# Performance work log

Hardware: AMD Instinct MI355X
Metric: run time of the kernel (lower is better)

Reference implementation:

```python
import jax, jax.numpy as jnp
import numpy as np

B, C_IN, C_OUT, N, T = 32, 64, 64, 1024, 16


def setup_inputs() -> dict:
    key = jax.random.key(0)
    k1, k2, k3, k4, k5 = jax.random.split(key, 5)
    x = jax.random.normal(k1, (B, C_IN, N, T), dtype=jnp.float32)
    adj = jax.random.uniform(k2, (N, N), dtype=jnp.float32)
    alpha = jax.random.normal(k3, (C_IN,), dtype=jnp.float32) * 0.1
    W_att = jax.random.normal(k4, (T, T), dtype=jnp.float32) * 0.1
    W_out = jax.random.normal(k5, (C_OUT, C_IN), dtype=jnp.float32) * 0.1
    return {"x": x, "adj": adj, "alpha": alpha, "W_att": W_att, "W_out": W_out}


def reference(x, adj, alpha, W_att, W_out):
    # x: [B, C_in, N, T]; adj: [N, N]
    # k = q = einsum('bint,i->bnt', x, alpha)
    k = jnp.einsum('bint,i->bnt', x, alpha)              # [B, N, T]
    # scores = k @ W @ q^T over timestep dim -> [B, N, N]
    scores = jnp.einsum('bnt,ts,bms->bnm', k, W_att, k)
    att = jax.nn.softmax(scores, axis=-1) * adj          # [B, N, N]
    # out = (att @ x.permute(3,0,2,1)) @ W_out.T, then permute back
    agg = jnp.einsum('bnm,bcmt->bcnt', att, x)           # [B, C_in, N, T]
    out = jnp.einsum('bcnt,oc->bont', agg, W_out)        # [B, C_out, N, T]
    return out
```

## Files before the change

### kernel.cpp

```cpp
#include <hip/hip_runtime.h>
#include <hip/hip_bf16.h>


typedef float  f32x4 __attribute__((ext_vector_type(4)));
typedef short  s16x8 __attribute__((ext_vector_type(8)));
typedef unsigned short u16x8 __attribute__((ext_vector_type(8)));

#define GLOAD_LDS16(g, l) __builtin_amdgcn_global_load_lds(                    \
    (const __attribute__((address_space(1))) void*)(g),                        \
    (__attribute__((address_space(3))) void*)(l), 16, 0, 0)

static __device__ __forceinline__ unsigned short f2bf(float f) {
    __hip_bfloat16 h = __float2bfloat16(f);
    return *reinterpret_cast<unsigned short*>(&h);
}

__global__ __launch_bounds__(256) void kCM(const float* __restrict__ x,
                                           const float* __restrict__ Wout,
                                           const float* __restrict__ alpha,
                                           const float* __restrict__ Watt,
                                           unsigned short* __restrict__ Yt,
                                           float* __restrict__ kk_,
                                           float* __restrict__ kq_) {
    extern __shared__ char sm[];
    float* xt = (float*)sm;
    unsigned short* Ys = (unsigned short*)sm;
    unsigned short* Wb = (unsigned short*)(sm + 66560);
    float* al = (float*)(sm + 75776);
    float* wl = (float*)(sm + 76032);
    float* kl = (float*)(sm + 77120);
    int tid = threadIdx.x;
    int b  = blockIdx.x >> 6;
    int mc = blockIdx.x & 63;
    int j0 = mc << 8;
    int m0 = mc << 4;
    if (tid < 64) al[tid] = alpha[tid];
    wl[(tid >> 4) * 17 + (tid & 15)] = Watt[tid];
    #pragma unroll
    for (int it = 0; it < 16; ++it) {
        int idx = it * 256 + tid;
        Wb[(idx >> 6) * 72 + (idx & 63)] = f2bf(Wout[idx]);
    }
    const float* xb = x + (size_t)b * (64 * 16384) + j0;
    #pragma unroll
    for (int it = 0; it < 16; ++it) {
        int idx = it * 256 + tid;
        int c = idx >> 6, j4 = (idx & 63) << 2;
        float4 v = *(const float4*)(xb + (size_t)c * 16384 + j4);
        *(float4*)&xt[c * 260 + j4] = v;
    }
    __syncthreads();
    int w = tid >> 6, l = tid & 63;
    int l15 = l & 15, lhi = l >> 4;
    int jw = w << 6;
    f32x4 acc[4][4] = {};
    s16x8 af[4][2];
    #pragma unroll
    for (int fro = 0; fro < 4; ++fro)
        #pragma unroll
        for (int ks = 0; ks < 2; ++ks)
            af[fro][ks] = *(const s16x8*)&Wb[(fro * 16 + l15) * 72 + ks * 32 + lhi * 8];
    #pragma unroll
    for (int fc = 0; fc < 4; ++fc) {
        #pragma unroll
        for (int ks = 0; ks < 2; ++ks) {
            int jcol = jw + fc * 16 + l15;
            int cb = ks * 32 + lhi * 8;
            s16x8 bf;
            #pragma unroll
            for (int e = 0; e < 8; ++e)
                bf[e] = (short)f2bf(xt[(cb + e) * 260 + jcol]);
            #pragma unroll
            for (int fro = 0; fro < 4; ++fro)
                acc[fro][fc] = __builtin_amdgcn_mfma_f32_16x16x32_bf16(
                    af[fro][ks], bf, acc[fro][fc], 0, 0, 0);
        }
    }
    {
        float kv = 0.f;
        #pragma unroll
        for (int c = 0; c < 64; ++c) kv = fmaf(al[c], xt[c * 260 + tid], kv);
        kl[tid] = kv;
        kk_[(size_t)b * 16384 + j0 + tid] = kv;
    }
    __syncthreads();
    {
        int ml = tid >> 4, tq = tid & 15;
        float q = 0.f;
        #pragma unroll
        for (int s = 0; s < 16; ++s) q = fmaf(kl[ml * 16 + s], wl[s * 17 + tq], q);
        kq_[(size_t)b * 16384 + j0 + tid] = q;
    }
    #pragma unroll
    for (int fro = 0; fro < 4; ++fro)
        #pragma unroll
        for (int fc = 0; fc < 4; ++fc) {
            int jl = jw + fc * 16 + l15;
            int o0 = fro * 16 + lhi * 4;
            ushort4 pk = make_ushort4(f2bf(acc[fro][fc][0]), f2bf(acc[fro][fc][1]),
                                      f2bf(acc[fro][fc][2]), f2bf(acc[fro][fc][3]));
            *(ushort4*)&Ys[jl * 72 + o0] = pk;
        }
    __syncthreads();
    #pragma unroll
    for (int it = 0; it < 4; ++it) {
        int r = it * 256 + tid;
        int o = r >> 4, t = r & 15;
        u16x8 v0, v1;
        #pragma unroll
        for (int q = 0; q < 8; ++q) {
            v0[q] = Ys[(q * 16 + t) * 72 + o];
            v1[q] = Ys[((q + 8) * 16 + t) * 72 + o];
        }
        unsigned short* dst = Yt + (((size_t)b << 10) + r) * 1024 + m0;
        *(u16x8*)dst = v0;
        *(u16x8*)(dst + 8) = v1;
    }
}

__global__ __launch_bounds__(256) void kBP(const float* __restrict__ kk_,
                                           const float* __restrict__ kq_,
                                           const float* __restrict__ adj,
                                           unsigned short* __restrict__ Pbf) {
    int tid = threadIdx.x;
    int b  = blockIdx.x >> 8;
    int n0 = (blockIdx.x & 255) * 4;
    __shared__ float kql[4][16];
    __shared__ float redm[4][4], reds[4][4];
    if (tid < 64)
        kql[tid >> 4][tid & 15] =
            kq_[((size_t)b * 1024 + n0 + (tid >> 4)) * 16 + (tid & 15)];
    __syncthreads();
    const float* kb = kk_ + (size_t)b * 16384;
    float kf[4][16];
    #pragma unroll
    for (int u = 0; u < 4; ++u) {
        const float* p = &kb[(size_t)(u * 256 + tid) * 16];
        #pragma unroll
        for (int s = 0; s < 16; ++s) kf[u][s] = p[s];
    }
    float sc[4][4];
    #pragma unroll
    for (int r = 0; r < 4; ++r)
        #pragma unroll
        for (int u = 0; u < 4; ++u) {
            float a = 0.f;
            #pragma unroll
            for (int s = 0; s < 16; ++s) a = fmaf(kql[r][s], kf[u][s], a);
            sc[r][u] = a;
        }
    float mx[4];
    #pragma unroll
    for (int r = 0; r < 4; ++r)
        mx[r] = fmaxf(fmaxf(sc[r][0], sc[r][1]), fmaxf(sc[r][2], sc[r][3]));
    #pragma unroll
    for (int off = 32; off; off >>= 1)
        #pragma unroll
        for (int r = 0; r < 4; ++r) mx[r] = fmaxf(mx[r], __shfl_xor(mx[r], off));
    int w = tid >> 6;
    if ((tid & 63) == 0)
        #pragma unroll
        for (int r = 0; r < 4; ++r) redm[w][r] = mx[r];
    __syncthreads();
    #pragma unroll
    for (int r = 0; r < 4; ++r)
        mx[r] = fmaxf(fmaxf(redm[0][r], redm[1][r]), fmaxf(redm[2][r], redm[3][r]));
    float e[4][4], se[4];
    #pragma unroll
    for (int r = 0; r < 4; ++r) {
        float s = 0.f;
        #pragma unroll
        for (int u = 0; u < 4; ++u) { e[r][u] = __expf(sc[r][u] - mx[r]); s += e[r][u]; }
        se[r] = s;
    }
    #pragma unroll
    for (int off = 32; off; off >>= 1)
        #pragma unroll
        for (int r = 0; r < 4; ++r) se[r] += __shfl_xor(se[r], off);
    if ((tid & 63) == 0)
        #pragma unroll
        for (int r = 0; r < 4; ++r) reds[w][r] = se[r];
    __syncthreads();
    float rrs[4];
    #pragma unroll
    for (int r = 0; r < 4; ++r)
        rrs[r] = 1.f / (reds[0][r] + reds[1][r] + reds[2][r] + reds[3][r]);
    #pragma unroll
    for (int r = 0; r < 4; ++r)
        #pragma unroll
        for (int u = 0; u < 4; ++u) {
            size_t m = (size_t)u * 256 + tid;
            float av = adj[(size_t)(n0 + r) * 1024 + m];
            Pbf[((size_t)b * 1024 + n0 + r) * 1024 + m] = f2bf(e[r][u] * rrs[r] * av);
        }
}

static __device__ __forceinline__ void stage32(const unsigned short* Pb,
                                               const unsigned short* Yb,
                                               unsigned short* lds, int buf,
                                               int kt, int ww, int l) {
    int S  = ((l >> 2) ^ (l >> 4)) & 3;
    int cs = (((l & 3) ^ S)) << 3;
    int k0 = kt << 5;
    unsigned short* base = lds + buf * 16384;
    #pragma unroll
    for (int s = 0; s < 2; ++s) {
        int rbase = s * 128 + ww * 16;
        size_t g = ((size_t)(rbase + (l >> 2)) << 10) + k0 + cs;
        GLOAD_LDS16(Pb + g, base + rbase * 32);
        GLOAD_LDS16(Yb + g, base + 8192 + rbase * 32);
    }
}

static __device__ __forceinline__ s16x8 frag32(const unsigned short* base,
                                               int row, int l) {
    int S = (row ^ (row >> 2)) & 3;
    int g = (l >> 4) & 3;
    return *(const s16x8*)(base + row * 32 + ((g ^ S) << 3));
}

__global__ __launch_bounds__(512, 2) void kD(const unsigned short* __restrict__ P,
                                             const unsigned short* __restrict__ Yt,
                                             float* __restrict__ out) {
    extern __shared__ unsigned short lds[];
    int bid = blockIdx.x;
    int wg  = (bid & 7) * 64 + (bid >> 3);
    int b   = wg >> 4;
    int rem = wg & 15;
    int n0  = (rem & 3) << 8;
    int j0  = (rem >> 2) << 8;
    int tid = threadIdx.x;
    int l = tid & 63, ww = tid >> 6;
    int wr = ww >> 2, wc = ww & 3;
    int l15 = l & 15, lhi = l >> 4;
    const unsigned short* Pb = P  + ((size_t)b << 20) + ((size_t)n0 << 10);
    const unsigned short* Yb = Yt + ((size_t)b << 20) + ((size_t)j0 << 10);

    f32x4 acc[8][4] = {};
    stage32(Pb, Yb, lds, 0, 0, ww, l);
    stage32(Pb, Yb, lds, 1, 1, ww, l);

    for (int kt = 0; kt < 32; ++kt) {
        int cur = kt % 3;
        const unsigned short* Ab = lds + cur * 16384;
        const unsigned short* Bb = Ab + 8192;
        if (kt < 31) asm volatile("s_waitcnt vmcnt(4)" ::: "memory");
        else         asm volatile("s_waitcnt vmcnt(0)" ::: "memory");
        __builtin_amdgcn_s_barrier();
        s16x8 bf[4], af0[4];
        #pragma unroll
        for (int nj = 0; nj < 4; ++nj)
            bf[nj] = frag32(Bb, wc * 64 + nj * 16 + l15, l);
        #pragma unroll
        for (int mi = 0; mi < 4; ++mi)
            af0[mi] = frag32(Ab, wr * 128 + mi * 16 + l15, l);
        if (kt < 30) stage32(Pb, Yb, lds, (kt + 2) % 3, kt + 2, ww, l);
        __builtin_amdgcn_s_barrier();
        asm volatile("s_waitcnt lgkmcnt(0)" ::: "memory");
        __builtin_amdgcn_sched_barrier(0);
        __builtin_amdgcn_s_setprio(1);
        #pragma unroll
        for (int mi = 0; mi < 4; ++mi)
            #pragma unroll
            for (int nj = 0; nj < 4; ++nj)
                acc[mi][nj] = __builtin_amdgcn_mfma_f32_16x16x32_bf16(
                    af0[mi], bf[nj], acc[mi][nj], 0, 0, 0);
        __builtin_amdgcn_s_setprio(0);
        __builtin_amdgcn_s_barrier();
        s16x8 af1[4];
        #pragma unroll
        for (int mi = 0; mi < 4; ++mi)
            af1[mi] = frag32(Ab, wr * 128 + (4 + mi) * 16 + l15, l);
        asm volatile("s_waitcnt lgkmcnt(0)" ::: "memory");
        __builtin_amdgcn_sched_barrier(0);
        __builtin_amdgcn_s_setprio(1);
        #pragma unroll
        for (int mi = 0; mi < 4; ++mi)
            #pragma unroll
            for (int nj = 0; nj < 4; ++nj)
                acc[4 + mi][nj] = __builtin_amdgcn_mfma_f32_16x16x32_bf16(
                    af1[mi], bf[nj], acc[4 + mi][nj], 0, 0, 0);
        __builtin_amdgcn_s_setprio(0);
    }

    #pragma unroll
    for (int mi = 0; mi < 8; ++mi)
        #pragma unroll
        for (int nj = 0; nj < 4; ++nj) {
            int o  = (j0 >> 4) + wc * 4 + nj;
            int nb = n0 + wr * 128 + mi * 16 + lhi * 4;
            float* op = out + ((size_t)(b * 64 + o) << 14) + (size_t)nb * 16 + l15;
            #pragma unroll
            for (int q = 0; q < 4; ++q) op[q * 16] = acc[mi][nj][q];
        }
}

extern "C" void kernel_launch(void* const* d_in, const int* in_sizes, int n_in,
                              void* d_out, int out_size, void* d_ws, size_t ws_size,
                              hipStream_t stream) {
    const float* x     = (const float*)d_in[0];
    const float* adj   = (const float*)d_in[1];
    const float* alpha = (const float*)d_in[2];
    const float* Watt  = (const float*)d_in[3];
    const float* Wout  = (const float*)d_in[4];
    float* out = (float*)d_out;

    char* ws = (char*)d_ws;
    float* k  = (float*)ws;
    float* kq = (float*)(ws + 2097152);
    unsigned short* Pbf = (unsigned short*)(ws + 4194304);
    unsigned short* Yt  = (unsigned short*)(ws + 4194304 + 67108864);

    kCM<<<2048, 256, 78144, stream>>>(x, Wout, alpha, Watt, Yt, k, kq);
    kBP<<<8192, 256, 0, stream>>>(k, kq, adj, Pbf);
    kD <<<512, 512, 98304, stream>>>(Pbf, Yt, out);
}
```

Baseline: 202.0 us.

## Store x as bf16 in LDS in kCM and switch kD to double-buffered K=64 tiles

kCM now converts x to bf16 once while loading it into LDS and accumulates the alpha-weighted k sum during the load. This shrinks shared memory so three blocks fit per CU, and the later conversion and 64-step reduction loop are gone. kD moves from a 3-stage pipeline with K=32 tiles to a 2-buffer scheme with K=64 tiles, a new XOR swizzle, and the next tile's load issued early in each iteration. LDS use in kD grows to 128KB, and the shallower pipeline may expose more load latency.

```diff
diff --git a/kernel.cpp b/kernel.cpp
--- a/kernel.cpp
+++ b/kernel.cpp
@@ -15,25 +15,27 @@
     return *reinterpret_cast<unsigned short*>(&h);
 }
 
-__global__ __launch_bounds__(256) void kCM(const float* __restrict__ x,
-                                           const float* __restrict__ Wout,
-                                           const float* __restrict__ alpha,
-                                           const float* __restrict__ Watt,
-                                           unsigned short* __restrict__ Yt,
-                                           float* __restrict__ kk_,
-                                           float* __restrict__ kq_) {
+__global__ __launch_bounds__(256, 3) void kCM(const float* __restrict__ x,
+                                              const float* __restrict__ Wout,
+                                              const float* __restrict__ alpha,
+                                              const float* __restrict__ Watt,
+                                              unsigned short* __restrict__ Yt,
+                                              float* __restrict__ kk_,
+                                              float* __restrict__ kq_) {
     extern __shared__ char sm[];
-    float* xt = (float*)sm;
-    unsigned short* Ys = (unsigned short*)sm;
-    unsigned short* Wb = (unsigned short*)(sm + 66560);
-    float* al = (float*)(sm + 75776);
-    float* wl = (float*)(sm + 76032);
-    float* kl = (float*)(sm + 77120);
+    unsigned short* xtb = (unsigned short*)sm;
+    unsigned short* Ys  = (unsigned short*)sm;
+    unsigned short* Wb  = (unsigned short*)(sm + 36864);
+    float* al   = (float*)(sm + 46080);
+    float* wl   = (float*)(sm + 46336);
+    float* kl   = (float*)(sm + 47424);
+    float* kred = (float*)(sm + 48448);
     int tid = threadIdx.x;
     int b  = blockIdx.x >> 6;
     int mc = blockIdx.x & 63;
     int j0 = mc << 8;
     int m0 = mc << 4;
+    int g = tid >> 6, lane = tid & 63;
     if (tid < 64) al[tid] = alpha[tid];
     wl[(tid >> 4) * 17 + (tid & 15)] = Watt[tid];
     #pragma unroll
@@ -41,49 +43,56 @@
         int idx = it * 256 + tid;
         Wb[(idx >> 6) * 72 + (idx & 63)] = f2bf(Wout[idx]);
     }
+    __syncthreads();
     const float* xb = x + (size_t)b * (64 * 16384) + j0;
+    float kp[4] = {0.f, 0.f, 0.f, 0.f};
     #pragma unroll
     for (int it = 0; it < 16; ++it) {
-        int idx = it * 256 + tid;
-        int c = idx >> 6, j4 = (idx & 63) << 2;
-        float4 v = *(const float4*)(xb + (size_t)c * 16384 + j4);
-        *(float4*)&xt[c * 260 + j4] = v;
-    }
-    __syncthreads();
-    int w = tid >> 6, l = tid & 63;
-    int l15 = l & 15, lhi = l >> 4;
-    int jw = w << 6;
-    f32x4 acc[4][4] = {};
-    s16x8 af[4][2];
+        int c = it * 4 + g;
+        float4 v = *(const float4*)(xb + (size_t)c * 16384 + lane * 4);
+        float a = al[c];
+        kp[0] = fmaf(a, v.x, kp[0]);
+        kp[1] = fmaf(a, v.y, kp[1]);
+        kp[2] = fmaf(a, v.z, kp[2]);
+        kp[3] = fmaf(a, v.w, kp[3]);
+        ushort4 pk = make_ushort4(f2bf(v.x), f2bf(v.y), f2bf(v.z), f2bf(v.w));
+        *(ushort4*)&xtb[c * 264 + lane * 4] = pk;
+    }
+    *(float4*)&kred[g * 256 + lane * 4] = make_float4(kp[0], kp[1], kp[2], kp[3]);
+    __syncthreads();
+    int l15 = lane & 15, lhi = lane >> 4;
+    int jw = g << 6;
+    s16x8 af[4][2], bfv[4][2];
     #pragma unroll
     for (int fro = 0; fro < 4; ++fro)
         #pragma unroll
         for (int ks = 0; ks < 2; ++ks)
             af[fro][ks] = *(const s16x8*)&Wb[(fro * 16 + l15) * 72 + ks * 32 + lhi * 8];
     #pragma unroll
-    for (int fc = 0; fc < 4; ++fc) {
+    for (int fc = 0; fc < 4; ++fc)
         #pragma unroll
         for (int ks = 0; ks < 2; ++ks) {
             int jcol = jw + fc * 16 + l15;
             int cb = ks * 32 + lhi * 8;
-            s16x8 bf;
+            s16x8 t;
             #pragma unroll
             for (int e = 0; e < 8; ++e)
-                bf[e] = (short)f2bf(xt[(cb + e) * 260 + jcol]);
+                t[e] = (short)xtb[(cb + e) * 264 + jcol];
+            bfv[fc][ks] = t;
+        }
+    float kv = kred[tid] + kred[256 + tid] + kred[512 + tid] + kred[768 + tid];
+    kl[tid] = kv;
+    kk_[(size_t)b * 16384 + j0 + tid] = kv;
+    __syncthreads();
+    f32x4 acc[4][4] = {};
+    #pragma unroll
+    for (int ks = 0; ks < 2; ++ks)
+        #pragma unroll
+        for (int fc = 0; fc < 4; ++fc)
             #pragma unroll
             for (int fro = 0; fro < 4; ++fro)
                 acc[fro][fc] = __builtin_amdgcn_mfma_f32_16x16x32_bf16(
-                    af[fro][ks], bf, acc[fro][fc], 0, 0, 0);
-        }
-    }
-    {
-        float kv = 0.f;
-        #pragma unroll
-        for (int c = 0; c < 64; ++c) kv = fmaf(al[c], xt[c * 260 + tid], kv);
-        kl[tid] = kv;
-        kk_[(size_t)b * 16384 + j0 + tid] = kv;
-    }
-    __syncthreads();
+                    af[fro][ks], bfv[fc][ks], acc[fro][fc], 0, 0, 0);
     {
         int ml = tid >> 4, tq = tid & 15;
         float q = 0.f;
@@ -195,28 +204,26 @@
         }
 }
 
-static __device__ __forceinline__ void stage32(const unsigned short* Pb,
-                                               const unsigned short* Yb,
-                                               unsigned short* lds, int buf,
-                                               int kt, int ww, int l) {
-    int S  = ((l >> 2) ^ (l >> 4)) & 3;
-    int cs = (((l & 3) ^ S)) << 3;
-    int k0 = kt << 5;
-    unsigned short* base = lds + buf * 16384;
-    #pragma unroll
-    for (int s = 0; s < 2; ++s) {
-        int rbase = s * 128 + ww * 16;
-        size_t g = ((size_t)(rbase + (l >> 2)) << 10) + k0 + cs;
-        GLOAD_LDS16(Pb + g, base + rbase * 32);
-        GLOAD_LDS16(Yb + g, base + 8192 + rbase * 32);
-    }
-}
-
-static __device__ __forceinline__ s16x8 frag32(const unsigned short* base,
-                                               int row, int l) {
-    int S = (row ^ (row >> 2)) & 3;
-    int g = (l >> 4) & 3;
-    return *(const s16x8*)(base + row * 32 + ((g ^ S) << 3));
+static __device__ __forceinline__ void stage_tile(const unsigned short* Pb,
+                                                  const unsigned short* Yb,
+                                                  unsigned short* lds, int buf,
+                                                  int kt, int ww, int l) {
+    int r8  = (l >> 3) & 7;
+    int glc = ((l & 7) ^ r8) << 3;
+    int k0  = kt << 6;
+    unsigned short* base = lds + buf * 32768;
+    #pragma unroll
+    for (int s = 0; s < 4; ++s) {
+        int row  = s * 64 + ww * 8;
+        size_t g = ((size_t)(row + r8) << 10) + k0 + glc;
+        GLOAD_LDS16(Pb + g, base + row * 64);
+        GLOAD_LDS16(Yb + g, base + 16384 + row * 64);
+    }
+}
+
+static __device__ __forceinline__ s16x8 frag_ld(const unsigned short* base,
+                                                int R, int kc, int l7) {
+    return *(const s16x8*)(base + R * 64 + ((kc ^ l7) << 3));
 }
 
 __global__ __launch_bounds__(512, 2) void kD(const unsigned short* __restrict__ P,
@@ -232,55 +239,54 @@
     int tid = threadIdx.x;
     int l = tid & 63, ww = tid >> 6;
     int wr = ww >> 2, wc = ww & 3;
-    int l15 = l & 15, lhi = l >> 4;
+    int l15 = l & 15, lhi = l >> 4, l7 = l & 7;
     const unsigned short* Pb = P  + ((size_t)b << 20) + ((size_t)n0 << 10);
     const unsigned short* Yb = Yt + ((size_t)b << 20) + ((size_t)j0 << 10);
 
     f32x4 acc[8][4] = {};
-    stage32(Pb, Yb, lds, 0, 0, ww, l);
-    stage32(Pb, Yb, lds, 1, 1, ww, l);
-
-    for (int kt = 0; kt < 32; ++kt) {
-        int cur = kt % 3;
-        const unsigned short* Ab = lds + cur * 16384;
-        const unsigned short* Bb = Ab + 8192;
-        if (kt < 31) asm volatile("s_waitcnt vmcnt(4)" ::: "memory");
-        else         asm volatile("s_waitcnt vmcnt(0)" ::: "memory");
-        __builtin_amdgcn_s_barrier();
-        s16x8 bf[4], af0[4];
-        #pragma unroll
-        for (int nj = 0; nj < 4; ++nj)
-            bf[nj] = frag32(Bb, wc * 64 + nj * 16 + l15, l);
-        #pragma unroll
-        for (int mi = 0; mi < 4; ++mi)
-            af0[mi] = frag32(Ab, wr * 128 + mi * 16 + l15, l);
-        if (kt < 30) stage32(Pb, Yb, lds, (kt + 2) % 3, kt + 2, ww, l);
-        __builtin_amdgcn_s_barrier();
-        asm volatile("s_waitcnt lgkmcnt(0)" ::: "memory");
-        __builtin_amdgcn_sched_barrier(0);
-        __builtin_amdgcn_s_setprio(1);
-        #pragma unroll
-        for (int mi = 0; mi < 4; ++mi)
-            #pragma unroll
-            for (int nj = 0; nj < 4; ++nj)
-                acc[mi][nj] = __builtin_amdgcn_mfma_f32_16x16x32_bf16(
-                    af0[mi], bf[nj], acc[mi][nj], 0, 0, 0);
-        __builtin_amdgcn_s_setprio(0);
-        __builtin_amdgcn_s_barrier();
-        s16x8 af1[4];
-        #pragma unroll
-        for (int mi = 0; mi < 4; ++mi)
-            af1[mi] = frag32(Ab, wr * 128 + (4 + mi) * 16 + l15, l);
-        asm volatile("s_waitcnt lgkmcnt(0)" ::: "memory");
-        __builtin_amdgcn_sched_barrier(0);
-        __builtin_amdgcn_s_setprio(1);
-        #pragma unroll
-        for (int mi = 0; mi < 4; ++mi)
-            #pragma unroll
-            for (int nj = 0; nj < 4; ++nj)
-                acc[4 + mi][nj] = __builtin_amdgcn_mfma_f32_16x16x32_bf16(
-                    af1[mi], bf[nj], acc[4 + mi][nj], 0, 0, 0);
-        __builtin_amdgcn_s_setprio(0);
+    stage_tile(Pb, Yb, lds, 0, 0, ww, l);
+    __syncthreads();
+
+    for (int kt = 0; kt < 16; ++kt) {
+        int cur = kt & 1;
+        const unsigned short* Ab = lds + cur * 32768;
+        const unsigned short* Bb = Ab + 16384;
+        s16x8 bf[4][2];
+        #pragma unroll
+        for (int q = 0; q < 4; ++q) {
+            if (q == 0) {
+                int ktn = kt < 15 ? kt + 1 : 15;
+                stage_tile(Pb, Yb, lds, cur ^ 1, ktn, ww, l);
+                #pragma unroll
+                for (int nj = 0; nj < 4; ++nj)
+                    #pragma unroll
+                    for (int ks = 0; ks < 2; ++ks)
+                        bf[nj][ks] = frag_ld(Bb, wc * 64 + nj * 16 + l15,
+                                             ks * 4 + lhi, l7);
+            }
+            s16x8 af[2][2];
+            #pragma unroll
+            for (int mi = 0; mi < 2; ++mi)
+                #pragma unroll
+                for (int ks = 0; ks < 2; ++ks)
+                    af[mi][ks] = frag_ld(Ab, wr * 128 + (q * 2 + mi) * 16 + l15,
+                                         ks * 4 + lhi, l7);
+            __builtin_amdgcn_s_barrier();
+            asm volatile("s_waitcnt lgkmcnt(0)" ::: "memory");
+            __builtin_amdgcn_sched_barrier(0);
+            __builtin_amdgcn_s_setprio(1);
+            #pragma unroll
+            for (int mi = 0; mi < 2; ++mi)
+                #pragma unroll
+                for (int nj = 0; nj < 4; ++nj)
+                    #pragma unroll
+                    for (int ks = 0; ks < 2; ++ks)
+                        acc[q * 2 + mi][nj] = __builtin_amdgcn_mfma_f32_16x16x32_bf16(
+                            af[mi][ks], bf[nj][ks], acc[q * 2 + mi][nj], 0, 0, 0);
+            __builtin_amdgcn_s_setprio(0);
+            if (q < 3) __builtin_amdgcn_s_barrier();
+        }
+        __syncthreads();
     }
 
     #pragma unroll
@@ -311,7 +317,7 @@
     unsigned short* Pbf = (unsigned short*)(ws + 4194304);
     unsigned short* Yt  = (unsigned short*)(ws + 4194304 + 67108864);
 
-    kCM<<<2048, 256, 78144, stream>>>(x, Wout, alpha, Watt, Yt, k, kq);
+    kCM<<<2048, 256, 52544, stream>>>(x, Wout, alpha, Watt, Yt, k, kq);
     kBP<<<8192, 256, 0, stream>>>(k, kq, adj, Pbf);
-    kD <<<512, 512, 98304, stream>>>(Pbf, Yt, out);
-}
+    kD <<<512, 512, 131072, stream>>>(Pbf, Yt, out);
+}
```

Measured after the change: 193.8 us. -4.1%, faster.
